# Performance work log

Measured on AMD Instinct MI355X. Metric: run time of the kernel, lower is better.

The kernel has to match this reference:

```python
import jax, jax.numpy as jnp
import numpy as np

NH = 8          # attention heads
TEMP = 2.0      # gumbel temperature


def _gumbel_softmax_hard(logits, key, temperature):
    # hard=True straight-through gumbel softmax (module is in eval mode)
    g = jax.random.gumbel(key, logits.shape, logits.dtype)
    y = jax.nn.softmax((logits + g) / temperature, axis=-1)
    y_hard = jax.nn.one_hot(jnp.argmax(y, axis=-1), logits.shape[-1], dtype=y.dtype)
    return y_hard - jax.lax.stop_gradient(y) + y


def _experts(x, w1, w2, w3):
    # SwiGLU FFN over all experts at once: x [T,C], w1/w3 [E,H,C], w2 [E,C,H] -> [T,E,C]
    h = jax.nn.silu(jnp.einsum('tc,ehc->teh', x, w1)) * jnp.einsum('tc,ehc->teh', x, w3)
    return jnp.einsum('teh,ech->tec', h, w2)


def _mha(q_in, kv_in, in_w, in_b, out_w, out_b):
    C = q_in.shape[-1]
    hd = C // NH
    q = q_in @ in_w[:C].T + in_b[:C]
    k = kv_in @ in_w[C:2 * C].T + in_b[C:2 * C]
    v = kv_in @ in_w[2 * C:].T + in_b[2 * C:]
    B, Tq, _ = q.shape
    Tk = k.shape[1]
    q = q.reshape(B, Tq, NH, hd)
    k = k.reshape(B, Tk, NH, hd)
    v = v.reshape(B, Tk, NH, hd)
    scale = jnp.asarray(1.0 / np.sqrt(hd), q.dtype)
    att = jax.nn.softmax(jnp.einsum('bqhd,bkhd->bhqk', q, k) * scale, axis=-1)
    o = jnp.einsum('bhqk,bkhd->bqhd', att, v).reshape(B, Tq, C)
    return o @ out_w.T + out_b


def setup_inputs() -> dict:
    key = jax.random.key(0)
    ks = jax.random.split(key, 20)
    B, T, S, C, E, H = 2, 2048, 77, 1024, 4, 2816
    p = lambda k, sh: jax.random.normal(k, sh, jnp.float32) * 0.02
    return {
        'x': jax.random.normal(ks[0], (B, T, C), jnp.float32),
        'time': jax.random.normal(ks[1], (B,), jnp.float32),
        'caption': jax.random.normal(ks[2], (B, S, C), jnp.float32),
        'language': jax.random.randint(ks[3], (B,), 0, 9),
        'lang_embed': p(ks[4], (9, C)),
        'lang_gate_w': p(ks[5], (E, C)),
        'lang_gate_b': jnp.zeros((E,), jnp.float32),
        'lang_w1': p(ks[6], (E, H, C)),
        'lang_w2': p(ks[7], (E, C, H)),
        'lang_w3': p(ks[8], (E, H, C)),
        'in_proj_w': p(ks[9], (3 * C, C)),
        'in_proj_b': jnp.zeros((3 * C,), jnp.float32),
        'out_proj_w': p(ks[10], (C, C)),
        'out_proj_b': jnp.zeros((C,), jnp.float32),
        'cap_gate_w': p(ks[11], (E, C)),
        'cap_gate_b': jnp.zeros((E,), jnp.float32),
        'cap_w1': p(ks[12], (E, H, C)),
        'cap_w2': p(ks[13], (E, C, H)),
        'cap_w3': p(ks[14], (E, H, C)),
    }


def reference(x, time, caption, language, lang_embed, lang_gate_w, lang_gate_b,
              lang_w1, lang_w2, lang_w3, in_proj_w, in_proj_b, out_proj_w, out_proj_b,
              cap_gate_w, cap_gate_b, cap_w1, cap_w2, cap_w3):
    B, T, C = x.shape
    x_flat = x.reshape(-1, C)                                   # [B*T, C]

    # language gating (one logit vector per batch element, repeated over T tokens)
    lang_emb = lang_embed[language]                             # [B, C]
    lang_logits = lang_emb @ lang_gate_w.T + lang_gate_b        # [B, E]
    lang_probs = _gumbel_softmax_hard(lang_logits, jax.random.key(1), TEMP)
    lang_probs = jnp.repeat(lang_probs, T, axis=0)              # [B*T, E]

    lang_outputs = _experts(x_flat, lang_w1, lang_w2, lang_w3)  # [B*T, E, C]
    first_out = (lang_outputs * lang_probs[:, :, None]).sum(axis=1)  # [B*T, C]
    first_reshaped = first_out.reshape(B, T, C)

    # cross attention against caption, then per-token caption gating
    cross = _mha(first_reshaped, caption, in_proj_w, in_proj_b, out_proj_w, out_proj_b)
    cross_flat = cross.reshape(-1, C)
    cap_logits = cross_flat @ cap_gate_w.T + cap_gate_b         # [B*T, E]
    cap_probs = _gumbel_softmax_hard(cap_logits, jax.random.key(2), TEMP)

    cap_outputs = _experts(first_out, cap_w1, cap_w2, cap_w3)   # [B*T, E, C]
    second_out = (cap_outputs * cap_probs[:, :, None]).sum(axis=1)

    total_out = (first_out + second_out).reshape(B, T, C)

    all_probs = jnp.concatenate([lang_probs, cap_probs], axis=1)  # [B*T, 2E]
    expert_usage = all_probs.mean(axis=0)
    loss = (expert_usage * jnp.log(expert_usage + 1e-10)).sum()
    return total_out, loss
```

## Files before the change

kernel.cpp:

```cpp
#include <hip/hip_runtime.h>
#include <stdint.h>

#define B_ 2
#define T_ 2048
#define S_ 77
#define C_ 1024
#define E_ 4
#define H_ 2816
#define NH_ 8
#define HD_ 128
#define N_ (B_*T_)
#define MAXGB (N_/128 + E_)
#define MAXGB2 (N_/256 + E_)
#define PEsz ((size_t)H_*C_)
#define CC_ ((size_t)C_*C_)

typedef _Float16 h8 __attribute__((ext_vector_type(8)));
typedef _Float16 h4 __attribute__((ext_vector_type(4)));
typedef float f4 __attribute__((ext_vector_type(4)));

__device__ __forceinline__ void gload16(const void* g, void* l){
  __builtin_amdgcn_global_load_lds((const __attribute__((address_space(1))) void*)g,
                                   (__attribute__((address_space(3))) void*)l, 16, 0, 0);
}

__device__ __forceinline__ void xcd_swizzle(int& bx, int& by){
  int nx = gridDim.x, ny = gridDim.y;
  int nwg = nx*ny;
  int wg = by*nx + bx;
  int q = nwg >> 3, r = nwg & 7;
  int xcd = wg & 7, idx = wg >> 3;
  int s = (xcd < r ? xcd*(q+1) : r*(q+1) + (xcd-r)*q) + idx;
  bx = s % nx; by = s / nx;
}

__device__ __forceinline__ uint32_t rotl32(uint32_t v, int r){ return (v<<r)|(v>>(32-r)); }
__device__ __forceinline__ void threefry2x32(uint32_t k0, uint32_t k1,
                                             uint32_t x, uint32_t y,
                                             uint32_t& o0, uint32_t& o1){
  uint32_t k2 = k0 ^ k1 ^ 0x1BD11BDAu;
  x += k0; y += k1;
#define TFR(r) { x += y; y = rotl32(y, r); y ^= x; }
  TFR(13) TFR(15) TFR(26) TFR(6)   x += k1; y += k2 + 1u;
  TFR(17) TFR(29) TFR(16) TFR(24)  x += k2; y += k0 + 2u;
  TFR(13) TFR(15) TFR(26) TFR(6)   x += k0; y += k1 + 3u;
  TFR(17) TFR(29) TFR(16) TFR(24)  x += k1; y += k2 + 4u;
  TFR(13) TFR(15) TFR(26) TFR(6)   x += k2; y += k0 + 5u;
#undef TFR
  o0 = x; o1 = y;
}
__device__ __forceinline__ float gumbel_from_bits(uint32_t bits){
  const float TINY = 1.17549435e-38f;
  float f = __uint_as_float((bits >> 9) | 0x3f800000u) - 1.0f;
  float u = fmaxf(TINY, f + TINY);
  return -logf(-logf(u));
}
__device__ __forceinline__ float jax_gumbel(uint32_t k0, uint32_t k1, uint32_t idx){
  uint32_t a, b;
  threefry2x32(k0, k1, 0u, idx, a, b);
  return gumbel_from_bits(a ^ b);
}

__device__ __forceinline__ void job_split(const float* __restrict__ s,
    _Float16* __restrict__ hi, _Float16* __restrict__ lo, long n4, int b0, int nb){
  for (long i = (long)b0*256 + threadIdx.x; i < n4; i += (long)nb*256){
    float4 v = ((const float4*)s)[i];
    h4 h, L;
    h[0]=(_Float16)v.x; h[1]=(_Float16)v.y; h[2]=(_Float16)v.z; h[3]=(_Float16)v.w;
    L[0]=(_Float16)(v.x-(float)h[0]); L[1]=(_Float16)(v.y-(float)h[1]);
    L[2]=(_Float16)(v.z-(float)h[2]); L[3]=(_Float16)(v.w-(float)h[3]);
    ((h4*)hi)[i] = h; ((h4*)lo)[i] = L;
  }
}
__device__ __forceinline__ void job_plain(const float* __restrict__ s,
    _Float16* __restrict__ d, long n4, int b0, int nb){
  for (long i = (long)b0*256 + threadIdx.x; i < n4; i += (long)nb*256){
    float4 v = ((const float4*)s)[i];
    h4 h;
    h[0]=(_Float16)v.x; h[1]=(_Float16)v.y; h[2]=(_Float16)v.z; h[3]=(_Float16)v.w;
    ((h4*)d)[i] = h;
  }
}
__device__ __forceinline__ void job_w13_plain(const float* __restrict__ w1,
    const float* __restrict__ w3, _Float16* __restrict__ dst, int nslot, int b0, int nb){
  const int K8 = C_/8;
  long total = (long)nslot * (2*H_) * K8;
  for (long i = (long)b0*256 + threadIdx.x; i < total; i += (long)nb*256){
    int kv = (int)(i & (K8-1));
    long rs = i >> 7;
    int r  = (int)(rs % (2*H_));
    int slot = (int)(rs / (2*H_));
    int gg = r >> 5, o = r & 31;
    const float* src = ((o<16)? w1 : w3) + (size_t)slot*PEsz + (size_t)(16*gg + (o&15))*C_ + kv*8;
    float4 v0 = *(const float4*)src, v1 = *(const float4*)(src+4);
    float vv[8] = {v0.x,v0.y,v0.z,v0.w,v1.x,v1.y,v1.z,v1.w};
    h8 hh;
#pragma unroll
    for (int jj=0;jj<8;++jj) hh[jj] = (_Float16)vv[jj];
    *(h8*)(dst + (size_t)slot*2*PEsz + (size_t)r*C_ + kv*8) = hh;
  }
}
__device__ __forceinline__ void job_w13_split_sel(const float* __restrict__ w1,
    const float* __restrict__ w3, int sel0, int sel1,
    _Float16* __restrict__ hi, _Float16* __restrict__ lo, int b0, int nb){
  const int K8 = C_/8;
  long total = 2L * (2*H_) * K8;
  for (long i = (long)b0*256 + threadIdx.x; i < total; i += (long)nb*256){
    int kv = (int)(i & (K8-1));
    long rs = i >> 7;
    int r  = (int)(rs % (2*H_));
    int slot = (int)(rs / (2*H_));
    int e = slot ? sel1 : sel0;
    int gg = r >> 5, o = r & 31;
    const float* src = ((o<16)? w1 : w3) + (size_t)e*PEsz + (size_t)(16*gg + (o&15))*C_ + kv*8;
    float4 v0 = *(const float4*)src, v1 = *(const float4*)(src+4);
    float vv[8] = {v0.x,v0.y,v0.z,v0.w,v1.x,v1.y,v1.z,v1.w};
    h8 hh, ll;
#pragma unroll
    for (int jj=0;jj<8;++jj){
      hh[jj] = (_Float16)vv[jj];
      ll[jj] = (_Float16)(vv[jj]-(float)hh[jj]);
    }
    size_t dof = (size_t)slot*2*PEsz + (size_t)r*C_ + kv*8;
    *(h8*)(hi + dof) = hh;
    *(h8*)(lo + dof) = ll;
  }
}
__device__ __forceinline__ void job_w2_split_sel(const float* __restrict__ w2,
    int sel0, int sel1, _Float16* __restrict__ hi, _Float16* __restrict__ lo, int b0, int nb){
  long per = (long)(PEsz/4);
  for (long i = (long)b0*256 + threadIdx.x; i < 2*per; i += (long)nb*256){
    int slot = (i >= per) ? 1 : 0;
    long ii = i - (long)slot*per;
    float4 v = ((const float4*)(w2 + (size_t)(slot?sel1:sel0)*PEsz))[ii];
    h4 h, L;
    h[0]=(_Float16)v.x; h[1]=(_Float16)v.y; h[2]=(_Float16)v.z; h[3]=(_Float16)v.w;
    L[0]=(_Float16)(v.x-(float)h[0]); L[1]=(_Float16)(v.y-(float)h[1]);
    L[2]=(_Float16)(v.z-(float)h[2]); L[3]=(_Float16)(v.w-(float)h[3]);
    ((h4*)(hi + (size_t)slot*PEsz))[ii] = h;
    ((h4*)(lo + (size_t)slot*PEsz))[ii] = L;
  }
}

#define CVA_W13 1024
#define CVA_W2  512
#define CVA_X   256
#define CVA_TOT (CVA_W13+CVA_W2+CVA_X)
__global__ __launch_bounds__(256) void convA(
    const float* __restrict__ lang_embed, const float* __restrict__ gate_w,
    const float* __restrict__ gate_b, const int* __restrict__ language,
    const float* __restrict__ w1, const float* __restrict__ w3, const float* __restrict__ w2,
    const float* __restrict__ x,
    _Float16* __restrict__ w13hi, _Float16* __restrict__ w13lo,
    _Float16* __restrict__ w2hi, _Float16* __restrict__ w2lo,
    _Float16* __restrict__ xhi, _Float16* __restrict__ xlo,
    float* __restrict__ langP, int* __restrict__ counts)
{
  __shared__ float lds8[8];
  const int tid = threadIdx.x, w = tid>>6, l = tid&63;
  for (int p = 2*w; p < 2*w+2; ++p){
    int b = p>>2, e = p&3;
    const float* emb = lang_embed + (size_t)language[b]*C_;
    const float* gw  = gate_w + (size_t)e*C_;
    float acc = 0.f;
    for (int c = l; c < C_; c += 64) acc += emb[c]*gw[c];
#pragma unroll
    for (int off = 32; off; off >>= 1) acc += __shfl_xor(acc, off);
    if (l == 0) lds8[p] = acc + gate_b[e];
  }
  __syncthreads();
  int sel[2];
  for (int b = 0; b < 2; ++b){
    float z[4], m = -3.4e38f;
    for (int e = 0; e < 4; ++e){
      float g = jax_gumbel(0u, 1u, (uint32_t)(b*4 + e));
      z[e] = (lds8[b*4 + e] + g) * 0.5f;
      m = fmaxf(m, z[e]);
    }
    float y[4], sum = 0.f;
    for (int e = 0; e < 4; ++e){ y[e] = expf(z[e]-m); sum += y[e]; }
    for (int e = 0; e < 4; ++e) y[e] = y[e] / sum;
    int best = 0; float bv = y[0];
    for (int e = 1; e < 4; ++e) if (y[e] > bv){ bv = y[e]; best = e; }
    sel[b] = best;
    if (blockIdx.x == 0 && tid == 0){
      for (int e = 0; e < 4; ++e)
        langP[b*4 + e] = ((e == best) ? 1.0f : 0.0f) - y[e] + y[e];
    }
  }
  if (blockIdx.x == 0 && tid == 0){
    for (int e = 0; e < 4; ++e) counts[e] = 0;
  }
  int bid = blockIdx.x;
  if (bid < CVA_W13)                 job_w13_split_sel(w1, w3, sel[0], sel[1], w13hi, w13lo, bid, CVA_W13);
  else if (bid < CVA_W13+CVA_W2)     job_w2_split_sel(w2, sel[0], sel[1], w2hi, w2lo, bid-CVA_W13, CVA_W2);
  else                               job_split(x, xhi, xlo, (long)((size_t)N_*C_/4), bid-CVA_W13-CVA_W2, CVA_X);
}

__global__ __launch_bounds__(512,2) void gemm_gate_split(
    const _Float16* __restrict__ Ahi, const _Float16* __restrict__ Alo,
    const _Float16* __restrict__ Bhi, const _Float16* __restrict__ Blo,
    _Float16* __restrict__ Hhi, _Float16* __restrict__ Hlo)
{
  __shared__ __align__(16) char smem[147456];
  const int tid = threadIdx.x, w = tid>>6, l = tid&63;
  const int lm = l&15, g = l>>4;
  const int wm = w>>1, wn = w&1;
  int bx = blockIdx.x, by = blockIdx.y;
  xcd_swizzle(bx, by);
  const int n0 = bx<<7;
  const int m0 = by<<8;
  const size_t eoff = (m0 >= T_) ? (size_t)2*PEsz : 0;

  const _Float16* srcA[4]; const _Float16* srcB[2];
#pragma unroll
  for (int jj=0;jj<4;++jj){
    int c = jj*512 + tid, r = c>>3, s = c&7;
    int st = s ^ (r&7);
    srcA[jj] = (st<4 ? Ahi : Alo) + (size_t)(m0 + r)*C_ + ((st&3)<<3);
  }
#pragma unroll
  for (int jj=0;jj<2;++jj){
    int c = jj*512 + tid, r = c>>3, s = c&7;
    int st = s ^ (r&7);
    srcB[jj] = (st<4 ? Bhi : Blo) + eoff + (size_t)(n0 + r)*C_ + ((st&3)<<3);
  }

#define STG(ts, bi) { \
    int k0 = (ts)<<5; \
    char* db = smem + (bi)*49152; \
    _Pragma("unroll") \
    for (int jj=0;jj<4;++jj) gload16(srcA[jj]+k0, db + (jj*512 + w*64)*16); \
    _Pragma("unroll") \
    for (int jj=0;jj<2;++jj) gload16(srcB[jj]+k0, db + 32768 + (jj*512 + w*64)*16); \
  }

  const int shi = (g ^ (lm&7)) << 4;
  int aoff[4], boff[4];
#pragma unroll
  for (int i=0;i<4;++i){
    aoff[i] = ((wm*64 + i*16 + lm)<<7) + shi;
    boff[i] = 32768 + ((wn*64 + i*16 + lm)<<7) + shi;
  }

  f4 acc[4][4] = {};
  const int nt = C_/32;
  STG(0,0) STG(1,1)
  for (int t=0; t<nt; ++t){
    const int bi = t%3;
    const int ts = (t+2 < nt) ? t+2 : 0;
    STG(ts, (t+2)%3)
    asm volatile("s_waitcnt vmcnt(12)" ::: "memory");
    __builtin_amdgcn_s_barrier();
    asm volatile("" ::: "memory");
    const char* base = smem + bi*49152;
    h8 ah[4], bh[4];
#pragma unroll
    for (int i=0;i<4;++i){ ah[i] = *(const h8*)(base + aoff[i]); bh[i] = *(const h8*)(base + boff[i]); }
    __builtin_amdgcn_s_setprio(1);
#pragma unroll
    for (int mi=0;mi<4;++mi)
#pragma unroll
      for (int ni=0;ni<4;++ni)
        acc[mi][ni] = __builtin_amdgcn_mfma_f32_16x16x32_f16(ah[mi], bh[ni], acc[mi][ni],0,0,0);
    __builtin_amdgcn_s_setprio(0);
    h8 bl[4];
#pragma unroll
    for (int i=0;i<4;++i) bl[i] = *(const h8*)(base + (boff[i]^64));
    __builtin_amdgcn_s_setprio(1);
#pragma unroll
    for (int mi=0;mi<4;++mi)
#pragma unroll
      for (int ni=0;ni<4;++ni)
        acc[mi][ni] = __builtin_amdgcn_mfma_f32_16x16x32_f16(ah[mi], bl[ni], acc[mi][ni],0,0,0);
    __builtin_amdgcn_s_setprio(0);
    h8 al[4];
#pragma unroll
    for (int i=0;i<4;++i) al[i] = *(const h8*)(base + (aoff[i]^64));
    __builtin_amdgcn_s_setprio(1);
#pragma unroll
    for (int mi=0;mi<4;++mi)
#pragma unroll
      for (int ni=0;ni<4;++ni)
        acc[mi][ni] = __builtin_amdgcn_mfma_f32_16x16x32_f16(al[mi], bh[ni], acc[mi][ni],0,0,0);
    __builtin_amdgcn_s_setprio(0);
    asm volatile("" ::: "memory");
    __builtin_amdgcn_s_barrier();
  }
#undef STG

#pragma unroll
  for (int mi=0;mi<4;++mi){
#pragma unroll
    for (int p=0;p<2;++p){
      int hc = ((n0 + wn*64)>>1) + p*16 + lm;
#pragma unroll
      for (int j=0;j<4;++j){
        int rl = wm*64 + mi*16 + (g<<2) + j;
        float s1 = acc[mi][2*p][j], s3 = acc[mi][2*p+1][j];
        float hval = s1/(1.f+expf(-s1))*s3;
        size_t row = (size_t)(m0 + rl);
        _Float16 hh = (_Float16)hval;
        Hhi[row*H_ + hc] = hh;
        Hlo[row*H_ + hc] = (_Float16)(hval - (float)hh);
      }
    }
  }
}

__global__ __launch_bounds__(512,2) void gemm_gate_plain(
    const _Float16* __restrict__ A, const _Float16* __restrict__ Bw,
    _Float16* __restrict__ Hout,
    const int* __restrict__ bmap_e, const int* __restrict__ bmap_s,
    const int* __restrict__ offs, const int* __restrict__ perm)
{
  __shared__ __align__(16) char smem[147456];
  const int tid = threadIdx.x, w = tid>>6, l = tid&63;
  const int lm = l&15, g = l>>4;
  const int wm = w>>1, wn = w&1;
  int bx = blockIdx.x, by = blockIdx.y;
  xcd_swizzle(bx, by);
  const int e = bmap_e[by]; if (e<0) return;
  const int m0 = bmap_s[by];
  int v = offs[e+1]-m0; const int valid = v>256?256:v;
  const size_t eoff = (size_t)e*2*PEsz;
  const int n0 = bx<<7;

  const _Float16* srcA[4]; const _Float16* srcB[2];
#pragma unroll
  for (int jj=0;jj<4;++jj){
    int c = jj*512 + tid, r = c>>3, s = c&7;
    int st = s ^ (r&7);
    int ia = m0 + r; ia = (ia<N_) ? ia : (N_-1);
    srcA[jj] = A + (size_t)perm[ia]*C_ + (st<<3);
  }
#pragma unroll
  for (int jj=0;jj<2;++jj){
    int c = jj*512 + tid, r = c>>3, s = c&7;
    int st = s ^ (r&7);
    srcB[jj] = Bw + eoff + (size_t)(n0 + r)*C_ + (st<<3);
  }

#define STG(ts, bi) { \
    int k0 = (ts)<<6; \
    char* db = smem + (bi)*49152; \
    _Pragma("unroll") \
    for (int jj=0;jj<4;++jj) gload16(srcA[jj]+k0, db + (jj*512 + w*64)*16); \
    _Pragma("unroll") \
    for (int jj=0;jj<2;++jj) gload16(srcB[jj]+k0, db + 32768 + (jj*512 + w*64)*16); \
  }

  const int shi = (g ^ (lm&7)) << 4;
  int aoff[4], boff[4];
#pragma unroll
  for (int i=0;i<4;++i){
    aoff[i] = ((wm*64 + i*16 + lm)<<7) + shi;
    boff[i] = 32768 + ((wn*64 + i*16 + lm)<<7) + shi;
  }

  f4 acc[4][4] = {};
  const int nt = C_/64;
  STG(0,0) STG(1,1)
  for (int t=0; t<nt; ++t){
    const int bi = t%3;
    const int ts = (t+2 < nt) ? t+2 : 0;
    STG(ts, (t+2)%3)
    asm volatile("s_waitcnt vmcnt(12)" ::: "memory");
    __builtin_amdgcn_s_barrier();
    asm volatile("" ::: "memory");
    const char* base = smem + bi*49152;
#pragma unroll
    for (int kk=0;kk<2;++kk){
      h8 af[4], bf[4];
      const int x = kk<<6;
#pragma unroll
      for (int i=0;i<4;++i){ af[i] = *(const h8*)(base + (aoff[i]^x)); bf[i] = *(const h8*)(base + (boff[i]^x)); }
      __builtin_amdgcn_s_setprio(1);
#pragma unroll
      for (int mi=0;mi<4;++mi)
#pragma unroll
        for (int ni=0;ni<4;++ni)
          acc[mi][ni] = __builtin_amdgcn_mfma_f32_16x16x32_f16(af[mi], bf[ni], acc[mi][ni],0,0,0);
      __builtin_amdgcn_s_setprio(0);
    }
    asm volatile("" ::: "memory");
    __builtin_amdgcn_s_barrier();
  }
#undef STG

#pragma unroll
  for (int mi=0;mi<4;++mi){
#pragma unroll
    for (int p=0;p<2;++p){
      int hc = ((n0 + wn*64)>>1) + p*16 + lm;
#pragma unroll
      for (int j=0;j<4;++j){
        int rl = wm*64 + mi*16 + (g<<2) + j;
        if (rl >= valid) continue;
        float s1 = acc[mi][2*p][j], s3 = acc[mi][2*p+1][j];
        Hout[(size_t)(m0 + rl)*H_ + hc] = (_Float16)(s1/(1.f+expf(-s1))*s3);
      }
    }
  }
}

template<int EPI, int NSEG, int EXPM>
__device__ __forceinline__ void gemm8_body(
    char* smem,
    const _Float16* __restrict__ A0, const _Float16* __restrict__ A1,
    const _Float16* __restrict__ B0, const _Float16* __restrict__ B1,
    const float* __restrict__ bias, float* __restrict__ Cf32,
    _Float16* __restrict__ O0, _Float16* __restrict__ O1,
    const int* __restrict__ bmap_e, const int* __restrict__ bmap_s,
    const int* __restrict__ offs, const int* __restrict__ perm,
    int M, int K, int Nw, size_t bstride_e, int bx, int by)
{
  const int tid = threadIdx.x, w = tid>>6, l = tid&63;
  const int lm = l&15, g = l>>4;
  const int wm = w>>1, wn = w&1;
  const int n0 = bx<<7;
  int m0, valid = 128; size_t eoff = 0;
  if constexpr (EXPM==3){
    int e = bmap_e[by]; if (e<0) return;
    m0 = bmap_s[by];
    int v = offs[e+1]-m0; valid = v>128?128:v;
    eoff = (size_t)e*bstride_e;
  } else {
    m0 = by<<7;
    if constexpr (EXPM==1) eoff = (m0>=T_) ? bstride_e : 0;
  }
  const int cAe = (((tid&7) ^ ((tid>>3)&7)) << 3);
  size_t rbA[4], rbB[4];
#pragma unroll
  for (int j=0;j<4;++j){
    int r = (j<<5) + (tid>>3);
    int ia = m0 + r;
    if constexpr (EXPM==3){ ia = (ia < N_) ? ia : (N_-1); }
    else { if (ia > M-1) ia = M-1; }
    rbA[j] = (size_t)ia*K + cAe;
    rbB[j] = eoff + (size_t)(n0+r)*K + cAe;
  }
  const int tps = K>>6, nt = NSEG*tps;

#define STAGE8(tt, cc) { \
    int sg = 0; \
    if constexpr (NSEG==3){ sg = ((tt)>=2*tps) ? 2 : (((tt)>=tps)?1:0); } \
    const _Float16* Asrc = (sg==1) ? A1 : A0; \
    const _Float16* Bsrc = (sg==2) ? B1 : B0; \
    int kk0 = ((tt) - sg*tps)<<6; \
    char* db = smem + (cc)*32768 + w*1024; \
    _Pragma("unroll") \
    for (int j=0;j<4;++j) gload16(Asrc + rbA[j] + kk0, db + j*4096); \
    _Pragma("unroll") \
    for (int j=0;j<4;++j) gload16(Bsrc + rbB[j] + kk0, db + 16384 + j*4096); \
  }

  int aoff[2][4], boff[2][4];
#pragma unroll
  for (int kk=0;kk<2;++kk){
#pragma unroll
    for (int i=0;i<4;++i){
      int ra = wm*64 + i*16 + lm;
      aoff[kk][i] = (ra<<7) + (((kk<<6)+(g<<4)) ^ ((ra&7)<<4));
      int rb = wn*64 + i*16 + lm;
      boff[kk][i] = (rb<<7) + (((kk<<6)+(g<<4)) ^ ((rb&7)<<4));
    }
  }

  f4 acc[4][4] = {};
  STAGE8(0, 0)
  for (int t=0; t<nt; ++t){
    const int c = t&1;
    if (t+1 < nt){
      STAGE8(t+1, c^1)
      asm volatile("s_waitcnt vmcnt(8)" ::: "memory");
    } else {
      asm volatile("s_waitcnt vmcnt(0)" ::: "memory");
    }
    __builtin_amdgcn_s_barrier();
    const char* Ab = smem + c*32768;
    const char* Bb = Ab + 16384;
#pragma unroll
    for (int kk=0;kk<2;++kk){
      h8 af[4], bf[4];
#pragma unroll
      for (int i=0;i<4;++i){
        af[i] = *(const h8*)(Ab + aoff[kk][i]);
        bf[i] = *(const h8*)(Bb + boff[kk][i]);
      }
      __builtin_amdgcn_s_setprio(1);
#pragma unroll
      for (int mi=0;mi<4;++mi)
#pragma unroll
        for (int ni=0;ni<4;++ni)
          acc[mi][ni] = __builtin_amdgcn_mfma_f32_16x16x32_f16(af[mi], bf[ni], acc[mi][ni],0,0,0);
      __builtin_amdgcn_s_setprio(0);
      __builtin_amdgcn_s_barrier();
    }
  }

#pragma unroll
  for (int mi=0;mi<4;++mi){
    const int rl0 = wm*64 + mi*16 + (g<<2);
#pragma unroll
    for (int ni=0;ni<4;++ni){
      int col = n0 + wn*64 + ni*16 + lm;
#pragma unroll
      for (int j=0;j<4;++j){
        int rl = rl0 + j;
        float vv = acc[mi][ni][j];
        if constexpr (EPI==0){
          int grow = m0 + rl;
          if (grow < M) Cf32[(size_t)grow*Nw + col] = vv + bias[col];
        } else if constexpr (EPI==1){
          int grow = m0 + rl;
          if (grow < M){
            float vb = vv + (bias ? bias[col] : 0.f);
            _Float16 hh = (_Float16)vb;
            O0[(size_t)grow*Nw + col] = hh;
            O1[(size_t)grow*Nw + col] = (_Float16)(vb - (float)hh);
          }
        } else {
          if (rl < valid){
            int orig = perm[m0 + rl];
            size_t o = (size_t)orig*C_ + col;
            Cf32[o] = (float)O0[o] + (float)O1[o] + vv;
          }
        }
      }
    }
  }
#undef STAGE8
}

template<int EPI, int NSEG, int EXPM>
__global__ __launch_bounds__(256,2) void gemm8(
    const _Float16* __restrict__ A0, const _Float16* __restrict__ A1,
    const _Float16* __restrict__ B0, const _Float16* __restrict__ B1,
    const float* __restrict__ bias, float* __restrict__ Cf32,
    _Float16* __restrict__ O0, _Float16* __restrict__ O1,
    const int* __restrict__ bmap_e, const int* __restrict__ bmap_s,
    const int* __restrict__ offs, const int* __restrict__ perm,
    int M, int K, int Nw, size_t bstride_e)
{
  __shared__ __align__(16) char smem[65536];
  int bx = blockIdx.x, by = blockIdx.y;
  xcd_swizzle(bx, by);
  gemm8_body<EPI,NSEG,EXPM>(smem, A0,A1,B0,B1,bias,Cf32,O0,O1,
                            bmap_e,bmap_s,offs,perm,M,K,Nw,bstride_e,bx,by);
}

__global__ __launch_bounds__(256,2) void ffn1_out_fused(
    const _Float16* __restrict__ Hbh, const _Float16* __restrict__ Hbl,
    const _Float16* __restrict__ w2hi, const _Float16* __restrict__ w2lo,
    _Float16* __restrict__ Fh, _Float16* __restrict__ Fl,
    const float* __restrict__ in_w, const float* __restrict__ out_w,
    const float* __restrict__ cap_w1, const float* __restrict__ cap_w3,
    const float* __restrict__ caption,
    _Float16* __restrict__ inwh, _Float16* __restrict__ inwl,
    _Float16* __restrict__ outwh, _Float16* __restrict__ outwl,
    _Float16* __restrict__ capw13,
    _Float16* __restrict__ caph, _Float16* __restrict__ capl)
{
  __shared__ __align__(16) char smem[65536];
  int id = blockIdx.x;
  if (id < 256){
    int s = (id&7)*32 + (id>>3);
    gemm8_body<1,3,1>(smem, Hbh, Hbl, w2hi, w2lo, nullptr, nullptr, Fh, Fl,
                      nullptr,nullptr,nullptr,nullptr, N_, H_, C_, PEsz, s&7, s>>3);
  } else {
    int cid = id - 256;
    if (cid < 320)      job_w13_plain(cap_w1, cap_w3, capw13, 4, cid, 320);
    else if (cid < 448) job_split(in_w, inwh, inwl, (long)(3*CC_/4), cid-320, 128);
    else if (cid < 496) job_split(out_w, outwh, outwl, (long)(CC_/4), cid-448, 48);
    else                job_split(caption, caph, capl, (long)((size_t)B_*S_*C_/4), cid-496, 16);
  }
}

__global__ __launch_bounds__(256,2) void gemm_qkv(
    const _Float16* __restrict__ Fh, const _Float16* __restrict__ Fl,
    const _Float16* __restrict__ caph, const _Float16* __restrict__ capl,
    const _Float16* __restrict__ inwh, const _Float16* __restrict__ inwl,
    const float* __restrict__ in_b,
    _Float16* __restrict__ Qh, _Float16* __restrict__ Ql,
    _Float16* __restrict__ KVh, _Float16* __restrict__ KVl,
    const float* __restrict__ cap_w2, _Float16* __restrict__ capw2f)
{
  __shared__ __align__(16) char smem[65536];
  int id = blockIdx.x;
  if (id < 256){
    int s = (id&7)*32 + (id>>3);
    gemm8_body<1,3,0>(smem, Fh, Fl, inwh, inwl, in_b, nullptr, Qh, Ql,
                      nullptr,nullptr,nullptr,nullptr, N_, C_, C_, 0, s&7, s>>3);
  } else if (id < 288){
    int cid = id - 256;
    gemm8_body<1,3,0>(smem, caph, capl, inwh + CC_, inwl + CC_, in_b + C_,
                      nullptr, KVh, KVl, nullptr,nullptr,nullptr,nullptr,
                      B_*S_, C_, 2*C_, 0, cid & 15, cid >> 4);
  } else {
    job_plain(cap_w2, capw2f, (long)(4*PEsz/4), id-288, 96);
  }
}

#define SP5 5
#define KSTR 136
#define VSTR 104
__global__ __launch_bounds__(256) void attn_mfma(
    const _Float16* __restrict__ Qh, const _Float16* __restrict__ Ql,
    const _Float16* __restrict__ KVh, const _Float16* __restrict__ KVl,
    _Float16* __restrict__ AOh, _Float16* __restrict__ AOl)
{
  __shared__ __align__(16) _Float16 Usm[2*128*VSTR];
  __shared__ __align__(16) _Float16 Psm[2*64*VSTR];
  _Float16* Kh_s = Usm;
  _Float16* Kl_s = Usm + 128*VSTR;
  _Float16* VTh  = Usm;
  _Float16* VTl  = Usm + 128*VSTR;
  _Float16* Ph   = Psm;
  _Float16* Pl   = Psm + 64*VSTR;

  const int tid = threadIdx.x;
  const int w = tid>>6, l = tid&63, lm = l&15, g = l>>4;
  const int b = blockIdx.z, h = blockIdx.y, q0 = blockIdx.x<<6;
  const float scale = 0.08838834764831845f;

  for (int i = tid; i < 64*VSTR; i += 256) ((uint32_t*)Psm)[i] = 0;
  {
    int oct = tid & 15, s0 = tid >> 4;
    for (int s = s0; s < 80; s += 16){
      h8 vh = {}, vl = {};
      if (s < S_){
        size_t ga = ((size_t)(b*S_ + s))*(2*C_) + h*HD_ + oct*8;
        vh = *(const h8*)(KVh + ga);
        vl = *(const h8*)(KVl + ga);
      }
      *(h8*)(Kh_s + s*KSTR + oct*8) = vh;
      *(h8*)(Kl_s + s*KSTR + oct*8) = vl;
    }
  }
  h8 qh[4], ql[4];
  {
    size_t qrow = (size_t)(b*T_ + q0 + w*16 + lm);
    const _Float16* qph = Qh + qrow*C_ + h*HD_ + g*8;
    const _Float16* qpl = Ql + qrow*C_ + h*HD_ + g*8;
#pragma unroll
    for (int ks=0; ks<4; ++ks){ qh[ks] = *(const h8*)(qph + ks*32); ql[ks] = *(const h8*)(qpl + ks*32); }
  }
  __syncthreads();

  f4 sc[SP5] = {};
#pragma unroll
  for (int ks=0; ks<4; ++ks){
#pragma unroll
    for (int nt=0; nt<SP5; ++nt){
      h8 kh = *(const h8*)(Kh_s + (nt*16+lm)*KSTR + ks*32 + g*8);
      h8 kl = *(const h8*)(Kl_s + (nt*16+lm)*KSTR + ks*32 + g*8);
      sc[nt] = __builtin_amdgcn_mfma_f32_16x16x32_f16(qh[ks], kh, sc[nt],0,0,0);
      sc[nt] = __builtin_amdgcn_mfma_f32_16x16x32_f16(ql[ks], kh, sc[nt],0,0,0);
      sc[nt] = __builtin_amdgcn_mfma_f32_16x16x32_f16(qh[ks], kl, sc[nt],0,0,0);
    }
  }

  float mx[4] = {-3e38f,-3e38f,-3e38f,-3e38f};
#pragma unroll
  for (int nt=0; nt<SP5; ++nt){
    bool valid = (nt*16+lm) < S_;
#pragma unroll
    for (int j=0;j<4;++j){
      float v = valid ? sc[nt][j]*scale : -3e38f;
      sc[nt][j] = v;
      mx[j] = fmaxf(mx[j], v);
    }
  }
#pragma unroll
  for (int off=1; off<16; off<<=1){
#pragma unroll
    for (int j=0;j<4;++j) mx[j] = fmaxf(mx[j], __shfl_xor(mx[j], off));
  }
  float sm[4] = {0,0,0,0};
#pragma unroll
  for (int nt=0; nt<SP5; ++nt){
    bool valid = (nt*16+lm) < S_;
#pragma unroll
    for (int j=0;j<4;++j){
      float p = valid ? expf(sc[nt][j]-mx[j]) : 0.f;
      sc[nt][j] = p; sm[j] += p;
    }
  }
#pragma unroll
  for (int off=1; off<16; off<<=1){
#pragma unroll
    for (int j=0;j<4;++j) sm[j] += __shfl_xor(sm[j], off);
  }
#pragma unroll
  for (int nt=0; nt<SP5; ++nt){
#pragma unroll
    for (int j=0;j<4;++j){
      int col = nt*16 + lm;
      if (col < S_){
        float p = sc[nt][j] / sm[j];
        int row = w*16 + g*4 + j;
        _Float16 ph = (_Float16)p;
        Ph[row*VSTR + col] = ph;
        Pl[row*VSTR + col] = (_Float16)(p - (float)ph);
      }
    }
  }
  __syncthreads();

  for (int i = tid; i < 128*VSTR; i += 256) ((uint32_t*)Usm)[i] = 0;
  __syncthreads();
  {
    int oct = tid & 15, s0 = tid >> 4;
    for (int s = s0; s < S_; s += 16){
      size_t ga = ((size_t)(b*S_ + s))*(2*C_) + C_ + h*HD_ + oct*8;
      h8 vh = *(const h8*)(KVh + ga);
      h8 vl = *(const h8*)(KVl + ga);
#pragma unroll
      for (int i2=0;i2<8;++i2){
        VTh[(oct*8+i2)*VSTR + s] = vh[i2];
        VTl[(oct*8+i2)*VSTR + s] = vl[i2];
      }
    }
  }
  __syncthreads();

  h8 pah[3], pal[3];
#pragma unroll
  for (int ks=0;ks<3;++ks){
    pah[ks] = *(const h8*)(Ph + (w*16+lm)*VSTR + ks*32 + g*8);
    pal[ks] = *(const h8*)(Pl + (w*16+lm)*VSTR + ks*32 + g*8);
  }
#pragma unroll
  for (int nt=0; nt<8; ++nt){
    f4 o = {};
#pragma unroll
    for (int ks=0;ks<3;++ks){
      h8 vh = *(const h8*)(VTh + (nt*16+lm)*VSTR + ks*32 + g*8);
      h8 vl = *(const h8*)(VTl + (nt*16+lm)*VSTR + ks*32 + g*8);
      o = __builtin_amdgcn_mfma_f32_16x16x32_f16(pah[ks], vh, o,0,0,0);
      o = __builtin_amdgcn_mfma_f32_16x16x32_f16(pal[ks], vh, o,0,0,0);
      o = __builtin_amdgcn_mfma_f32_16x16x32_f16(pah[ks], vl, o,0,0,0);
    }
#pragma unroll
    for (int j=0;j<4;++j){
      size_t orow = (size_t)(b*T_ + q0 + w*16 + g*4 + j);
      size_t oa = orow*C_ + h*HD_ + nt*16 + lm;
      _Float16 hh = (_Float16)o[j];
      AOh[oa] = hh;
      AOl[oa] = (_Float16)(o[j] - (float)hh);
    }
  }
}

__global__ __launch_bounds__(256) void cap_gate(
    const float* __restrict__ CR, const float* __restrict__ gw, const float* __restrict__ gb,
    int* __restrict__ cap_sel, float* __restrict__ capP, int* __restrict__ counts)
{
  int tid = threadIdx.x, wave = tid >> 6, lane = tid & 63;
  for (int r = 0; r < 2; ++r){
    int row = (blockIdx.x << 3) + (wave << 1) + r;
    const float* xp = CR + (size_t)row * C_;
    float lg[E_];
#pragma unroll
    for (int e = 0; e < E_; ++e){
      const float* wv = gw + (size_t)e * C_;
      float p = 0.f;
      for (int c = lane; c < C_; c += 64) p += xp[c] * wv[c];
#pragma unroll
      for (int off = 32; off; off >>= 1) p += __shfl_xor(p, off);
      lg[e] = p + gb[e];
    }
    if (lane == 0){
      float z[E_], m = -3.4e38f;
      for (int e = 0; e < E_; ++e){
        float gmb = jax_gumbel(0u, 2u, (uint32_t)(row*E_ + e));
        z[e] = (lg[e] + gmb) * 0.5f;
        m = fmaxf(m, z[e]);
      }
      float y[E_], sum = 0.f;
      for (int e = 0; e < E_; ++e){ y[e] = expf(z[e] - m); sum += y[e]; }
      for (int e = 0; e < E_; ++e) y[e] = y[e] / sum;
      int best = 0; float bv = y[0];
      for (int e = 1; e < E_; ++e) if (y[e] > bv){ bv = y[e]; best = e; }
      cap_sel[row] = best;
      atomicAdd(&counts[best], 1);
      for (int e = 0; e < E_; ++e)
        capP[(size_t)row*E_ + e] = ((e == best) ? 1.0f : 0.0f) - y[e] + y[e];
    }
  }
}

__global__ __launch_bounds__(256) void finalize(
    const int* __restrict__ counts, const int* __restrict__ cap_sel,
    int* __restrict__ offs,
    int* __restrict__ bmap_e, int* __restrict__ bmap_s,
    int* __restrict__ bmap_e2, int* __restrict__ bmap_s2,
    int* __restrict__ perm,
    const float* __restrict__ capP, const float* __restrict__ langP,
    float* __restrict__ out_loss)
{
  __shared__ int loffs[5];
  __shared__ int lcur[4];
  __shared__ float red[4][256];
  int tid = threadIdx.x;
  if (blockIdx.x == 0){
    if (tid == 0){
      loffs[0] = 0;
      for (int e = 0; e < E_; ++e){ loffs[e+1] = loffs[e] + counts[e]; lcur[e] = loffs[e]; }
      for (int e = 0; e < E_+1; ++e) offs[e] = loffs[e];
      int idx = 0;
      for (int e = 0; e < E_; ++e)
        for (int s = loffs[e]; s < loffs[e+1]; s += 128){ bmap_e[idx] = e; bmap_s[idx] = s; ++idx; }
      for (; idx < MAXGB; ++idx) bmap_e[idx] = -1;
      int idx2 = 0;
      for (int e = 0; e < E_; ++e)
        for (int s = loffs[e]; s < loffs[e+1]; s += 256){ bmap_e2[idx2] = e; bmap_s2[idx2] = s; ++idx2; }
      for (; idx2 < MAXGB2; ++idx2) bmap_e2[idx2] = -1;
    }
    __syncthreads();
    for (int row = tid; row < N_; row += 256){
      int e = cap_sel[row];
      int pos = atomicAdd(&lcur[e], 1);
      perm[pos] = row;
    }
  } else {
    float p0=0.f, p1=0.f, p2=0.f, p3=0.f;
    for (int r = tid; r < N_; r += 256){
      const float* p = capP + (size_t)r*E_;
      p0 += p[0]; p1 += p[1]; p2 += p[2]; p3 += p[3];
    }
    red[0][tid]=p0; red[1][tid]=p1; red[2][tid]=p2; red[3][tid]=p3;
    __syncthreads();
    for (int s = 128; s > 0; s >>= 1){
      if (tid < s){
        red[0][tid]+=red[0][tid+s]; red[1][tid]+=red[1][tid+s];
        red[2][tid]+=red[2][tid+s]; red[3][tid]+=red[3][tid+s];
      }
      __syncthreads();
    }
    if (tid == 0){
      float loss = 0.f;
      for (int e = 0; e < E_; ++e){
        float ul = (langP[e] + langP[E_ + e]) * 0.5f;
        loss += ul * logf(ul + 1e-10f);
      }
      for (int e = 0; e < E_; ++e){
        float uc = red[e][0] * (1.0f / N_);
        loss += uc * logf(uc + 1e-10f);
      }
      out_loss[0] = loss;
    }
  }
}

extern "C" void kernel_launch(void* const* d_in, const int* in_sizes, int n_in,
                              void* d_out, int out_size, void* d_ws, size_t ws_size,
                              hipStream_t stream)
{
  const float* x          = (const float*)d_in[0];
  const float* caption    = (const float*)d_in[2];
  const int*   language   = (const int*)  d_in[3];
  const float* lang_embed = (const float*)d_in[4];
  const float* lang_gw    = (const float*)d_in[5];
  const float* lang_gb    = (const float*)d_in[6];
  const float* lang_w1    = (const float*)d_in[7];
  const float* lang_w2    = (const float*)d_in[8];
  const float* lang_w3    = (const float*)d_in[9];
  const float* in_w       = (const float*)d_in[10];
  const float* in_b       = (const float*)d_in[11];
  const float* out_w      = (const float*)d_in[12];
  const float* out_b      = (const float*)d_in[13];
  const float* cap_gw     = (const float*)d_in[14];
  const float* cap_gb     = (const float*)d_in[15];
  const float* cap_w1     = (const float*)d_in[16];
  const float* cap_w2     = (const float*)d_in[17];
  const float* cap_w3     = (const float*)d_in[18];
  float* out = (float*)d_out;

  const size_t NC = (size_t)N_*C_;
  const size_t NHe = (size_t)N_*H_;
  const size_t KVel = (size_t)B_*S_*2*C_;
  const size_t CAPel = (size_t)B_*S_*C_;

  char* base = (char*)d_ws;
  size_t cur = 0;
  auto alloc = [&](size_t bytes)->char*{
    char* p = base + cur;
    cur += (bytes + 255) & ~(size_t)255;
    return p;
  };
  float* Qcross = (float*)alloc(NC*4);
  _Float16* Qh = (_Float16*)Qcross;
  _Float16* Ql = Qh + NC;
  char* kvreg = alloc(KVel*4);
  _Float16* KVh = (_Float16*)kvreg;
  _Float16* KVl = KVh + KVel;
  float* capP   = (float*)alloc((size_t)N_*E_*4);
  float* langP  = (float*)alloc(64);
  int* lang_sel = (int*)alloc(64);
  int* cap_sel  = (int*)alloc(N_*4);
  int* counts   = (int*)alloc(64);
  int* offs     = (int*)alloc(64);
  int* cursor   = (int*)alloc(64);
  int* bmap_e   = (int*)alloc(MAXGB*4);
  int* bmap_s   = (int*)alloc(MAXGB*4);
  int* bmap_e2  = (int*)alloc(MAXGB2*4);
  int* bmap_s2  = (int*)alloc(MAXGB2*4);
  int* perm     = (int*)alloc(N_*4);
  _Float16* xAO_hi = (_Float16*)alloc(NC*2);
  _Float16* xAO_lo = (_Float16*)alloc(NC*2);
  _Float16* cap_hi = (_Float16*)alloc(CAPel*2);
  _Float16* cap_lo = (_Float16*)alloc(CAPel*2);
  _Float16* Hb_hi  = (_Float16*)alloc(NHe*2);
  _Float16* Hb_lo  = (_Float16*)alloc(NHe*2);
  _Float16* F_hi   = (_Float16*)alloc(NC*2);
  _Float16* F_lo   = (_Float16*)alloc(NC*2);
  _Float16* Wreg = (_Float16*)alloc(2*( (size_t)3*CC_*2 + CC_*2 + 3*4*PEsz ));
  _Float16* w13hi = Wreg;
  _Float16* w13lo = Wreg + 4*PEsz;
  _Float16* w2hi  = Wreg + 8*PEsz;
  _Float16* w2lo  = Wreg + 10*PEsz;
  _Float16* capw13f = Wreg;
  _Float16* capw2f  = Wreg + 8*PEsz;
  _Float16* inw_hi  = Wreg + 12*PEsz;
  _Float16* inw_lo  = inw_hi + 3*CC_;
  _Float16* outw_hi = inw_lo + 3*CC_;
  _Float16* outw_lo = outw_hi + CC_;
  (void)lang_sel; (void)cursor;

  convA<<<CVA_TOT, 256, 0, stream>>>(
      lang_embed, lang_gw, lang_gb, language,
      lang_w1, lang_w3, lang_w2, x,
      w13hi, w13lo, w2hi, w2lo, xAO_hi, xAO_lo, langP, counts);

  gemm_gate_split<<<dim3((2*H_)/128, N_/256), 512, 0, stream>>>(
      xAO_hi, xAO_lo, w13hi, w13lo, Hb_hi, Hb_lo);

  ffn1_out_fused<<<768, 256, 0, stream>>>(
      Hb_hi, Hb_lo, w2hi, w2lo, F_hi, F_lo,
      in_w, out_w, cap_w1, cap_w3, caption,
      inw_hi, inw_lo, outw_hi, outw_lo, capw13f, cap_hi, cap_lo);

  gemm_qkv<<<384, 256, 0, stream>>>(
      F_hi, F_lo, cap_hi, cap_lo, inw_hi, inw_lo, in_b,
      Qh, Ql, KVh, KVl, cap_w2, capw2f);

  attn_mfma<<<dim3(T_/64, NH_, B_), 256, 0, stream>>>(Qh, Ql, KVh, KVl, xAO_hi, xAO_lo);

  gemm8<0,3,0><<<dim3(C_/128, N_/128), 256, 0, stream>>>(
      xAO_hi, xAO_lo, outw_hi, outw_lo, out_b, Qcross, nullptr, nullptr,
      nullptr, nullptr, nullptr, nullptr, N_, C_, C_, 0);

  cap_gate<<<N_/8, 256, 0, stream>>>(Qcross, cap_gw, cap_gb, cap_sel, capP, counts);

  finalize<<<2, 256, 0, stream>>>(counts, cap_sel, offs, bmap_e, bmap_s,
                                  bmap_e2, bmap_s2, perm, capP, langP, out + NC);

  _Float16* H2 = Hb_hi;
  gemm_gate_plain<<<dim3((2*H_)/128, MAXGB2), 512, 0, stream>>>(
      F_hi, capw13f, H2, bmap_e2, bmap_s2, offs, perm);

  gemm8<2,1,3><<<dim3(C_/128, MAXGB), 256, 0, stream>>>(
      H2, nullptr, capw2f, nullptr, nullptr, out, F_hi, F_lo,
      bmap_e, bmap_s, offs, perm, N_, H_, C_, PEsz);
}
```

Before: 690.6 us.

## Fold out-projection into caption gate weights and drop the out_proj GEMM

Because the cross-attention output feeds only the caption gate logits, the out-projection and the gate projection are folded algebraically into a 4xC weight (cap_gw @ out_w) plus a bias term, computed in spare blocks of the QKV kernel. The full NxCxC out_proj GEMM and its fp32 intermediate go away, and cap_gate now reads the fp16 hi/lo attention output directly. The cap_w2 conversion work moves into extra blocks of the attention kernel, and the XCD swizzle changes to column-major tile order. Summing in a different order can shift the gate logits slightly and could flip an argmax near a tie.

```diff
diff --git a/kernel.cpp b/kernel.cpp
--- a/kernel.cpp
+++ b/kernel.cpp
@@ -24,14 +24,14 @@
                                    (__attribute__((address_space(3))) void*)l, 16, 0, 0);
 }
 
-__device__ __forceinline__ void xcd_swizzle(int& bx, int& by){
+__device__ __forceinline__ void xcd_swizzle_cm(int& bx, int& by){
   int nx = gridDim.x, ny = gridDim.y;
   int nwg = nx*ny;
   int wg = by*nx + bx;
   int q = nwg >> 3, r = nwg & 7;
   int xcd = wg & 7, idx = wg >> 3;
   int s = (xcd < r ? xcd*(q+1) : r*(q+1) + (xcd-r)*q) + idx;
-  bx = s % nx; by = s / nx;
+  bx = s / ny; by = s % ny;
 }
 
 __device__ __forceinline__ uint32_t rotl32(uint32_t v, int r){ return (v<<r)|(v>>(32-r)); }
@@ -141,6 +141,25 @@
     ((h4*)(lo + (size_t)slot*PEsz))[ii] = L;
   }
 }
+__device__ __forceinline__ void job_foldw(const float* __restrict__ outw,
+    const float* __restrict__ capgw, const float* __restrict__ outb,
+    float* __restrict__ Wp, float* __restrict__ bp, int b0){
+  int e = b0 >> 2;
+  int k = ((b0 & 3) << 8) + threadIdx.x;
+  const float* cg = capgw + e*C_;
+  float acc = 0.f;
+  for (int c = 0; c < C_; ++c) acc += cg[c] * outw[(size_t)c*C_ + k];
+  Wp[e*C_ + k] = acc;
+  if ((b0 & 3) == 0){
+    int wv = threadIdx.x >> 6, l = threadIdx.x & 63;
+    const float* cg2 = capgw + wv*C_;
+    float a2 = 0.f;
+    for (int c = l; c < C_; c += 64) a2 += outb[c] * cg2[c];
+#pragma unroll
+    for (int off = 32; off; off >>= 1) a2 += __shfl_xor(a2, off);
+    if (l == 0 && e == 0) bp[wv] = a2;
+  }
+}
 
 #define CVA_W13 1024
 #define CVA_W2  512
@@ -207,7 +226,7 @@
   const int lm = l&15, g = l>>4;
   const int wm = w>>1, wn = w&1;
   int bx = blockIdx.x, by = blockIdx.y;
-  xcd_swizzle(bx, by);
+  xcd_swizzle_cm(bx, by);
   const int n0 = bx<<7;
   const int m0 = by<<8;
   const size_t eoff = (m0 >= T_) ? (size_t)2*PEsz : 0;
@@ -319,7 +338,7 @@
   const int lm = l&15, g = l>>4;
   const int wm = w>>1, wn = w&1;
   int bx = blockIdx.x, by = blockIdx.y;
-  xcd_swizzle(bx, by);
+  xcd_swizzle_cm(bx, by);
   const int e = bmap_e[by]; if (e<0) return;
   const int m0 = bmap_s[by];
   int v = offs[e+1]-m0; const int valid = v>256?256:v;
@@ -509,10 +528,7 @@
       for (int j=0;j<4;++j){
         int rl = rl0 + j;
         float vv = acc[mi][ni][j];
-        if constexpr (EPI==0){
-          int grow = m0 + rl;
-          if (grow < M) Cf32[(size_t)grow*Nw + col] = vv + bias[col];
-        } else if constexpr (EPI==1){
+        if constexpr (EPI==1){
           int grow = m0 + rl;
           if (grow < M){
             float vb = vv + (bias ? bias[col] : 0.f);
@@ -545,7 +561,7 @@
 {
   __shared__ __align__(16) char smem[65536];
   int bx = blockIdx.x, by = blockIdx.y;
-  xcd_swizzle(bx, by);
+  xcd_swizzle_cm(bx, by);
   gemm8_body<EPI,NSEG,EXPM>(smem, A0,A1,B0,B1,bias,Cf32,O0,O1,
                             bmap_e,bmap_s,offs,perm,M,K,Nw,bstride_e,bx,by);
 }
@@ -554,25 +570,22 @@
     const _Float16* __restrict__ Hbh, const _Float16* __restrict__ Hbl,
     const _Float16* __restrict__ w2hi, const _Float16* __restrict__ w2lo,
     _Float16* __restrict__ Fh, _Float16* __restrict__ Fl,
-    const float* __restrict__ in_w, const float* __restrict__ out_w,
+    const float* __restrict__ in_w,
     const float* __restrict__ cap_w1, const float* __restrict__ cap_w3,
     const float* __restrict__ caption,
     _Float16* __restrict__ inwh, _Float16* __restrict__ inwl,
-    _Float16* __restrict__ outwh, _Float16* __restrict__ outwl,
     _Float16* __restrict__ capw13,
     _Float16* __restrict__ caph, _Float16* __restrict__ capl)
 {
   __shared__ __align__(16) char smem[65536];
   int id = blockIdx.x;
   if (id < 256){
-    int s = (id&7)*32 + (id>>3);
     gemm8_body<1,3,1>(smem, Hbh, Hbl, w2hi, w2lo, nullptr, nullptr, Fh, Fl,
-                      nullptr,nullptr,nullptr,nullptr, N_, H_, C_, PEsz, s&7, s>>3);
+                      nullptr,nullptr,nullptr,nullptr, N_, H_, C_, PEsz, id&7, id>>3);
   } else {
     int cid = id - 256;
-    if (cid < 320)      job_w13_plain(cap_w1, cap_w3, capw13, 4, cid, 320);
-    else if (cid < 448) job_split(in_w, inwh, inwl, (long)(3*CC_/4), cid-320, 128);
-    else if (cid < 496) job_split(out_w, outwh, outwl, (long)(CC_/4), cid-448, 48);
+    if (cid < 352)      job_w13_plain(cap_w1, cap_w3, capw13, 4, cid, 352);
+    else if (cid < 496) job_split(in_w, inwh, inwl, (long)(3*CC_/4), cid-352, 144);
     else                job_split(caption, caph, capl, (long)((size_t)B_*S_*C_/4), cid-496, 16);
   }
 }
@@ -584,34 +597,37 @@
     const float* __restrict__ in_b,
     _Float16* __restrict__ Qh, _Float16* __restrict__ Ql,
     _Float16* __restrict__ KVh, _Float16* __restrict__ KVl,
-    const float* __restrict__ cap_w2, _Float16* __restrict__ capw2f)
+    const float* __restrict__ out_w, const float* __restrict__ cap_gw,
+    const float* __restrict__ out_b, float* __restrict__ Wp, float* __restrict__ bp)
 {
   __shared__ __align__(16) char smem[65536];
   int id = blockIdx.x;
   if (id < 256){
-    int s = (id&7)*32 + (id>>3);
     gemm8_body<1,3,0>(smem, Fh, Fl, inwh, inwl, in_b, nullptr, Qh, Ql,
-                      nullptr,nullptr,nullptr,nullptr, N_, C_, C_, 0, s&7, s>>3);
+                      nullptr,nullptr,nullptr,nullptr, N_, C_, C_, 0, id&7, id>>3);
   } else if (id < 288){
     int cid = id - 256;
     gemm8_body<1,3,0>(smem, caph, capl, inwh + CC_, inwl + CC_, in_b + C_,
                       nullptr, KVh, KVl, nullptr,nullptr,nullptr,nullptr,
                       B_*S_, C_, 2*C_, 0, cid & 15, cid >> 4);
   } else {
-    job_plain(cap_w2, capw2f, (long)(4*PEsz/4), id-288, 96);
+    job_foldw(out_w, cap_gw, out_b, Wp, bp, id-288);
   }
 }
 
 #define SP5 5
 #define KSTR 136
 #define VSTR 104
-__global__ __launch_bounds__(256) void attn_mfma(
+__global__ __launch_bounds__(256) void attn_fused(
     const _Float16* __restrict__ Qh, const _Float16* __restrict__ Ql,
     const _Float16* __restrict__ KVh, const _Float16* __restrict__ KVl,
-    _Float16* __restrict__ AOh, _Float16* __restrict__ AOl)
+    _Float16* __restrict__ AOh, _Float16* __restrict__ AOl,
+    const float* __restrict__ cap_w2, _Float16* __restrict__ capw2f)
 {
   __shared__ __align__(16) _Float16 Usm[2*128*VSTR];
   __shared__ __align__(16) _Float16 Psm[2*64*VSTR];
+  int id = blockIdx.x;
+  if (id >= 512){ job_plain(cap_w2, capw2f, (long)(4*PEsz/4), id-512, 128); return; }
   _Float16* Kh_s = Usm;
   _Float16* Kl_s = Usm + 128*VSTR;
   _Float16* VTh  = Usm;
@@ -621,7 +637,7 @@
 
   const int tid = threadIdx.x;
   const int w = tid>>6, l = tid&63, lm = l&15, g = l>>4;
-  const int b = blockIdx.z, h = blockIdx.y, q0 = blockIdx.x<<6;
+  const int b = id >> 8, h = (id >> 5) & 7, q0 = (id & 31) << 6;
   const float scale = 0.08838834764831845f;
 
   for (int i = tid; i < 64*VSTR; i += 256) ((uint32_t*)Psm)[i] = 0;
@@ -754,22 +770,30 @@
 }
 
 __global__ __launch_bounds__(256) void cap_gate(
-    const float* __restrict__ CR, const float* __restrict__ gw, const float* __restrict__ gb,
+    const _Float16* __restrict__ AOh, const _Float16* __restrict__ AOl,
+    const float* __restrict__ Wp, const float* __restrict__ bp,
+    const float* __restrict__ gb,
     int* __restrict__ cap_sel, float* __restrict__ capP, int* __restrict__ counts)
 {
   int tid = threadIdx.x, wave = tid >> 6, lane = tid & 63;
   for (int r = 0; r < 2; ++r){
     int row = (blockIdx.x << 3) + (wave << 1) + r;
-    const float* xp = CR + (size_t)row * C_;
+    float av[16];
+#pragma unroll
+    for (int i = 0; i < 16; ++i){
+      int c = lane + (i << 6);
+      av[i] = (float)AOh[(size_t)row*C_ + c] + (float)AOl[(size_t)row*C_ + c];
+    }
     float lg[E_];
 #pragma unroll
     for (int e = 0; e < E_; ++e){
-      const float* wv = gw + (size_t)e * C_;
+      const float* wv = Wp + (size_t)e * C_;
       float p = 0.f;
-      for (int c = lane; c < C_; c += 64) p += xp[c] * wv[c];
+#pragma unroll
+      for (int i = 0; i < 16; ++i) p += av[i] * wv[lane + (i << 6)];
 #pragma unroll
       for (int off = 32; off; off >>= 1) p += __shfl_xor(p, off);
-      lg[e] = p + gb[e];
+      lg[e] = p + bp[e] + gb[e];
     }
     if (lane == 0){
       float z[E_], m = -3.4e38f;
@@ -890,19 +914,18 @@
     cur += (bytes + 255) & ~(size_t)255;
     return p;
   };
-  float* Qcross = (float*)alloc(NC*4);
-  _Float16* Qh = (_Float16*)Qcross;
-  _Float16* Ql = Qh + NC;
+  _Float16* Qh = (_Float16*)alloc(NC*2);
+  _Float16* Ql = (_Float16*)alloc(NC*2);
   char* kvreg = alloc(KVel*4);
   _Float16* KVh = (_Float16*)kvreg;
   _Float16* KVl = KVh + KVel;
   float* capP   = (float*)alloc((size_t)N_*E_*4);
   float* langP  = (float*)alloc(64);
-  int* lang_sel = (int*)alloc(64);
+  float* Wp     = (float*)alloc(E_*C_*4);
+  float* bp     = (float*)alloc(64);
   int* cap_sel  = (int*)alloc(N_*4);
   int* counts   = (int*)alloc(64);
   int* offs     = (int*)alloc(64);
-  int* cursor   = (int*)alloc(64);
   int* bmap_e   = (int*)alloc(MAXGB*4);
   int* bmap_s   = (int*)alloc(MAXGB*4);
   int* bmap_e2  = (int*)alloc(MAXGB2*4);
@@ -925,9 +948,6 @@
   _Float16* capw2f  = Wreg + 8*PEsz;
   _Float16* inw_hi  = Wreg + 12*PEsz;
   _Float16* inw_lo  = inw_hi + 3*CC_;
-  _Float16* outw_hi = inw_lo + 3*CC_;
-  _Float16* outw_lo = outw_hi + CC_;
-  (void)lang_sel; (void)cursor;
 
   convA<<<CVA_TOT, 256, 0, stream>>>(
       lang_embed, lang_gw, lang_gb, language,
@@ -939,20 +959,16 @@
 
   ffn1_out_fused<<<768, 256, 0, stream>>>(
       Hb_hi, Hb_lo, w2hi, w2lo, F_hi, F_lo,
-      in_w, out_w, cap_w1, cap_w3, caption,
-      inw_hi, inw_lo, outw_hi, outw_lo, capw13f, cap_hi, cap_lo);
-
-  gemm_qkv<<<384, 256, 0, stream>>>(
+      in_w, cap_w1, cap_w3, caption,
+      inw_hi, inw_lo, capw13f, cap_hi, cap_lo);
+
+  gemm_qkv<<<304, 256, 0, stream>>>(
       F_hi, F_lo, cap_hi, cap_lo, inw_hi, inw_lo, in_b,
-      Qh, Ql, KVh, KVl, cap_w2, capw2f);
-
-  attn_mfma<<<dim3(T_/64, NH_, B_), 256, 0, stream>>>(Qh, Ql, KVh, KVl, xAO_hi, xAO_lo);
-
-  gemm8<0,3,0><<<dim3(C_/128, N_/128), 256, 0, stream>>>(
-      xAO_hi, xAO_lo, outw_hi, outw_lo, out_b, Qcross, nullptr, nullptr,
-      nullptr, nullptr, nullptr, nullptr, N_, C_, C_, 0);
-
-  cap_gate<<<N_/8, 256, 0, stream>>>(Qcross, cap_gw, cap_gb, cap_sel, capP, counts);
+      Qh, Ql, KVh, KVl, out_w, cap_gw, out_b, Wp, bp);
+
+  attn_fused<<<640, 256, 0, stream>>>(Qh, Ql, KVh, KVl, xAO_hi, xAO_lo, cap_w2, capw2f);
+
+  cap_gate<<<N_/8, 256, 0, stream>>>(xAO_hi, xAO_lo, Wp, bp, cap_gb, cap_sel, capP, counts);
 
   finalize<<<2, 256, 0, stream>>>(counts, cap_sel, offs, bmap_e, bmap_s,
                                   bmap_e2, bmap_s2, perm, capP, langP, out + NC);
```

Result: faster. 660.1 us (-4.4%).
